# Optimization experiments

Measured on AMD Instinct MI355X. Metric: run time of the kernel, lower is better.

Reference implementation:

```python
import jax, jax.numpy as jnp
import numpy as np

D_MODEL = 1024
D_STATE = 16
D_CONV = 4
EXPAND = 2
D_INNER = D_MODEL * EXPAND
LN_EPS = 1e-5


def setup_inputs() -> dict:
    key = jax.random.key(0)
    ks = jax.random.split(key, 12)
    s = lambda fan_in: 1.0 / np.sqrt(fan_in)
    return {
        "x": jax.random.normal(ks[0], (4, 2048, D_MODEL), dtype=jnp.float32),
        "ln_w": jnp.ones((D_MODEL,), jnp.float32),
        "ln_b": jnp.zeros((D_MODEL,), jnp.float32),
        "W_in": jax.random.uniform(ks[1], (D_MODEL, 2 * D_INNER), jnp.float32, -s(D_MODEL), s(D_MODEL)),
        "b_in": jax.random.uniform(ks[2], (2 * D_INNER,), jnp.float32, -s(D_MODEL), s(D_MODEL)),
        "conv_w": jax.random.uniform(ks[3], (D_INNER, 1, D_CONV), jnp.float32, -s(D_CONV), s(D_CONV)),
        "conv_b": jax.random.uniform(ks[4], (D_INNER,), jnp.float32, -s(D_CONV), s(D_CONV)),
        "A_log": jax.random.normal(ks[5], (D_INNER, D_STATE), jnp.float32),
        "D": jax.random.normal(ks[6], (D_INNER,), jnp.float32),
        "W_x": jax.random.uniform(ks[7], (D_INNER, 2 * D_STATE), jnp.float32, -s(D_INNER), s(D_INNER)),
        "b_x": jax.random.uniform(ks[8], (2 * D_STATE,), jnp.float32, -s(D_INNER), s(D_INNER)),
        "W_out": jax.random.uniform(ks[9], (D_INNER, D_MODEL), jnp.float32, -s(D_INNER), s(D_INNER)),
        "b_out": jax.random.uniform(ks[10], (D_MODEL,), jnp.float32, -s(D_INNER), s(D_INNER)),
    }


def _selective_scan(xc, deltaA, Bm, Cm):
    # xc: (b, s, di), deltaA: (di, n), Bm/Cm: (b, s, n)
    b, _, di = xc.shape
    n = Bm.shape[-1]
    h0 = jnp.zeros((b, di, n), xc.dtype)

    def step(h, inp):
        xt, bt, ct = inp  # (b,di), (b,n), (b,n)
        h = deltaA[None] * h + xt[:, :, None] * bt[:, None, :]
        y = jnp.einsum('bin,bn->bi', h, ct)
        return h, y

    xs = (jnp.swapaxes(xc, 0, 1), jnp.swapaxes(Bm, 0, 1), jnp.swapaxes(Cm, 0, 1))
    _, ys = jax.lax.scan(step, h0, xs)  # ys: (s, b, di)
    return jnp.swapaxes(ys, 0, 1)


def reference(x, ln_w, ln_b, W_in, b_in, conv_w, conv_b, A_log, D, W_x, b_x, W_out, b_out):
    residual = x
    mu = jnp.mean(x, -1, keepdims=True)
    var = jnp.mean((x - mu) ** 2, -1, keepdims=True)
    xn = (x - mu) * jax.lax.rsqrt(var + LN_EPS) * ln_w + ln_b
    xg = xn @ W_in + b_in
    x_main, gate = jnp.split(xg, 2, axis=-1)  # (b,s,di) each
    # causal depthwise conv1d (left pad d_conv-1 == torch pad both + slice [:s])
    xt = jnp.swapaxes(x_main, 1, 2)  # (b, di, s)
    xc = jax.lax.conv_general_dilated(
        xt, conv_w, window_strides=(1,), padding=[(D_CONV - 1, 0)],
        feature_group_count=D_INNER, dimension_numbers=('NCH', 'OIH', 'NCH'))
    xc = xc + conv_b[None, :, None]
    x_conv = jax.nn.silu(jnp.swapaxes(xc, 1, 2))  # (b,s,di)
    ssm = x_conv @ W_x + b_x
    Bm, Cm = jnp.split(ssm, 2, axis=-1)  # (b,s,n)
    deltaA = jnp.exp(-jnp.exp(A_log))  # exp(A), A = -exp(A_log)
    y = _selective_scan(x_conv, deltaA, Bm, Cm)
    y = y + x_conv * D[None, None, :]
    y = y * jax.nn.silu(gate)
    out = y @ W_out + b_out
    return out + residual
```

## Files before the change

### kernel.cpp

```cpp
#include <hip/hip_runtime.h>
#include <stdint.h>

typedef unsigned short u16;
typedef short bf16x8 __attribute__((ext_vector_type(8)));
typedef float f32x4 __attribute__((ext_vector_type(4)));

#define TOKENS 8192
#define SEQ 2048
#define DM 1024
#define DI 2048
#define NCH 32
#define CLEN 64

__device__ __forceinline__ float bf2f(u16 u) {
  union { uint32_t i; float f; } v; v.i = ((uint32_t)u) << 16; return v.f;
}
__device__ __forceinline__ u16 f2bf(float f) {
  union { float f; uint32_t i; } v; v.f = f;
  uint32_t r = v.i + 0x7FFFu + ((v.i >> 16) & 1u);
  return (u16)(r >> 16);
}

__device__ __forceinline__ void g2lds16(const void* g, void* l) {
  __builtin_amdgcn_global_load_lds(
      (const __attribute__((address_space(1))) uint32_t*)g,
      (__attribute__((address_space(3))) uint32_t*)l, 16, 0, 0);
}

__global__ __launch_bounds__(256)
void transpose_to_bf16(const float* __restrict__ src, u16* __restrict__ dst,
                       int R, int C) {
  __shared__ float tile[64][65];
  const int i = threadIdx.x;
  const int tilesC = C >> 6;
  const int br = blockIdx.x / tilesC, bc = blockIdx.x % tilesC;
  const int r0 = br << 6, c0 = bc << 6;
  const int cx = (i & 15) << 2, ry = i >> 4;
#pragma unroll
  for (int p = 0; p < 4; ++p) {
    int row = ry + p * 16;
    float4 v = *(const float4*)&src[(size_t)(r0 + row) * C + c0 + cx];
    tile[row][cx + 0] = v.x; tile[row][cx + 1] = v.y;
    tile[row][cx + 2] = v.z; tile[row][cx + 3] = v.w;
  }
  __syncthreads();
#pragma unroll
  for (int p = 0; p < 4; ++p) {
    int cr = ry + p * 16;
    ushort4 o;
    o.x = f2bf(tile[cx + 0][cr]); o.y = f2bf(tile[cx + 1][cr]);
    o.z = f2bf(tile[cx + 2][cr]); o.w = f2bf(tile[cx + 3][cr]);
    *(ushort4*)&dst[(size_t)(c0 + cr) * R + r0 + cx] = o;
  }
}

__global__ __launch_bounds__(256)
void txpose_wx(const float* __restrict__ src, u16* __restrict__ dst) {
  const int gid = blockIdx.x * 256 + threadIdx.x;
  const int k = gid >> 5, n = gid & 31;
  dst[(size_t)n * DI + k] = f2bf(src[gid]);
}

__global__ __launch_bounds__(256)
void layernorm_bf16(const float* __restrict__ x, const float* __restrict__ lw,
                    const float* __restrict__ lb, u16* __restrict__ xn) {
  const int row = blockIdx.x, tid = threadIdx.x;
  const float4 v = *(const float4*)&x[(size_t)row * DM + tid * 4];
  float s = v.x + v.y + v.z + v.w;
  float q = v.x * v.x + v.y * v.y + v.z * v.z + v.w * v.w;
#pragma unroll
  for (int m = 1; m < 64; m <<= 1) { s += __shfl_xor(s, m); q += __shfl_xor(q, m); }
  __shared__ float red[8];
  const int w = tid >> 6, lane = tid & 63;
  if (lane == 0) { red[w] = s; red[4 + w] = q; }
  __syncthreads();
  s = red[0] + red[1] + red[2] + red[3];
  q = red[4] + red[5] + red[6] + red[7];
  const float mu = s * (1.f / DM);
  const float var = q * (1.f / DM) - mu * mu;
  const float rs = rsqrtf(var + 1e-5f);
  const float4 wv = *(const float4*)&lw[tid * 4];
  const float4 bv = *(const float4*)&lb[tid * 4];
  ushort4 o;
  o.x = f2bf((v.x - mu) * rs * wv.x + bv.x);
  o.y = f2bf((v.y - mu) * rs * wv.y + bv.y);
  o.z = f2bf((v.z - mu) * rs * wv.z + bv.z);
  o.w = f2bf((v.w - mu) * rs * wv.w + bv.w);
  *(ushort4*)&xn[(size_t)row * DM + tid * 4] = o;
}

template <int EPI>
__global__ __launch_bounds__(256)
void gemm_bt(const u16* __restrict__ A, const u16* __restrict__ Bt,
             const float* __restrict__ bias, const float* __restrict__ resid,
             void* __restrict__ out, int M, int N, int K) {
  __shared__ __align__(16) u16 As[128 * 64];
  __shared__ __align__(16) u16 Bs[128 * 64];
  const int tid = threadIdx.x, w = tid >> 6, lane = tid & 63;
  const int ntiles = N >> 7;
  const int tm = blockIdx.x / ntiles, tn = blockIdx.x % ntiles;
  const int m0 = tm << 7, n0 = tn << 7;
  f32x4 acc[4][4];
#pragma unroll
  for (int mi = 0; mi < 4; ++mi)
#pragma unroll
    for (int ni = 0; ni < 4; ++ni) acc[mi][ni] = (f32x4){0.f, 0.f, 0.f, 0.f};

  const int chunkbase = w * 64 + lane;
  const int wm = (w >> 1) * 64, wn = (w & 1) * 64;
  const int fr = lane & 15, fg = lane >> 4;

  for (int kt = 0; kt < K; kt += 64) {
#pragma unroll
    for (int i = 0; i < 4; ++i) {
      int ch = chunkbase + i * 256;
      int row = ch >> 3, c16 = ch & 7;
      g2lds16(A + (size_t)(m0 + row) * K + kt + c16 * 8,
              (u16*)As + (size_t)(w * 64 + i * 256) * 8);
      g2lds16(Bt + (size_t)(n0 + row) * K + kt + c16 * 8,
              (u16*)Bs + (size_t)(w * 64 + i * 256) * 8);
    }
    __syncthreads();
#pragma unroll
    for (int ks = 0; ks < 2; ++ks) {
      bf16x8 af[4], bfr[4];
#pragma unroll
      for (int mi = 0; mi < 4; ++mi)
        af[mi] = *(const bf16x8*)&As[(wm + mi * 16 + fr) * 64 + ks * 32 + fg * 8];
#pragma unroll
      for (int ni = 0; ni < 4; ++ni)
        bfr[ni] = *(const bf16x8*)&Bs[(wn + ni * 16 + fr) * 64 + ks * 32 + fg * 8];
#pragma unroll
      for (int mi = 0; mi < 4; ++mi)
#pragma unroll
        for (int ni = 0; ni < 4; ++ni)
          acc[mi][ni] = __builtin_amdgcn_mfma_f32_16x16x32_bf16(
              af[mi], bfr[ni], acc[mi][ni], 0, 0, 0);
    }
    __syncthreads();
  }
#pragma unroll
  for (int mi = 0; mi < 4; ++mi)
#pragma unroll
    for (int ni = 0; ni < 4; ++ni) {
      const int col = n0 + wn + ni * 16 + fr;
      const float bcol = bias[col];
#pragma unroll
      for (int j = 0; j < 4; ++j) {
        const int row = m0 + wm + mi * 16 + fg * 4 + j;
        float v = acc[mi][ni][j] + bcol;
        if (EPI == 1) {
          ((float*)out)[(size_t)row * N + col] = v + resid[(size_t)row * N + col];
        } else {
          ((u16*)out)[(size_t)row * N + col] = f2bf(v);
        }
      }
    }
}

__global__ __launch_bounds__(256)
void conv_silu(const u16* __restrict__ xg, const float* __restrict__ cw,
               const float* __restrict__ cb, u16* __restrict__ xconv) {
  const int t = blockIdx.x;
  const int s = t & (SEQ - 1);
  const int d = threadIdx.x * 8;
  float xv[4][8];
#pragma unroll
  for (int j = 0; j < 4; ++j) {
    const int ss = s - 3 + j;
    if (ss >= 0) {
      uint4 u = *(const uint4*)&xg[(size_t)(t - 3 + j) * (2 * DI) + d];
      const u16* pu = (const u16*)&u;
#pragma unroll
      for (int q = 0; q < 8; ++q) xv[j][q] = bf2f(pu[q]);
    } else {
#pragma unroll
      for (int q = 0; q < 8; ++q) xv[j][q] = 0.f;
    }
  }
  u16 outp[8];
#pragma unroll
  for (int q = 0; q < 8; ++q) {
    const float4 wq = *(const float4*)&cw[(d + q) * 4];
    float a = cb[d + q] + wq.x * xv[0][q] + wq.y * xv[1][q] + wq.z * xv[2][q] +
              wq.w * xv[3][q];
    outp[q] = f2bf(a / (1.f + __expf(-a)));
  }
  *(uint4*)&xconv[(size_t)t * DI + d] = *(const uint4*)outp;
}

__global__ __launch_bounds__(256)
void bc_gemm(const u16* __restrict__ xconv, const u16* __restrict__ wxT,
             float* __restrict__ BCp) {
  __shared__ __align__(16) u16 As[128 * 64];
  __shared__ __align__(16) u16 Bs[32 * 64];
  const int tid = threadIdx.x, w = tid >> 6, lane = tid & 63;
  const int mt = blockIdx.x & 63;
  const int ks_id = blockIdx.x >> 6;
  const int m0 = mt << 7;
  const int k0 = ks_id << 9;
  const int fr = lane & 15, fg = lane >> 4;
  f32x4 acc[2][2];
#pragma unroll
  for (int mf = 0; mf < 2; ++mf)
#pragma unroll
    for (int nf = 0; nf < 2; ++nf) acc[mf][nf] = (f32x4){0.f, 0.f, 0.f, 0.f};

  for (int kt = k0; kt < k0 + 512; kt += 64) {
#pragma unroll
    for (int i = 0; i < 4; ++i) {
      int ch = w * 64 + lane + i * 256;
      int row = ch >> 3, c16 = ch & 7;
      g2lds16(xconv + (size_t)(m0 + row) * DI + kt + c16 * 8,
              (u16*)As + (size_t)(w * 64 + i * 256) * 8);
    }
    {
      int row = tid >> 3, c16 = tid & 7;
      g2lds16(wxT + (size_t)row * DI + kt + c16 * 8,
              (u16*)Bs + (size_t)(w * 64) * 8);
    }
    __syncthreads();
#pragma unroll
    for (int ks = 0; ks < 2; ++ks) {
      bf16x8 af[2], bfr[2];
#pragma unroll
      for (int mf = 0; mf < 2; ++mf)
        af[mf] = *(const bf16x8*)&As[(w * 32 + mf * 16 + fr) * 64 + ks * 32 + fg * 8];
#pragma unroll
      for (int nf = 0; nf < 2; ++nf)
        bfr[nf] = *(const bf16x8*)&Bs[(nf * 16 + fr) * 64 + ks * 32 + fg * 8];
#pragma unroll
      for (int mf = 0; mf < 2; ++mf)
#pragma unroll
        for (int nf = 0; nf < 2; ++nf)
          acc[mf][nf] = __builtin_amdgcn_mfma_f32_16x16x32_bf16(
              af[mf], bfr[nf], acc[mf][nf], 0, 0, 0);
    }
    __syncthreads();
  }
#pragma unroll
  for (int mf = 0; mf < 2; ++mf)
#pragma unroll
    for (int nf = 0; nf < 2; ++nf) {
      const int col = nf * 16 + fr;
#pragma unroll
      for (int j = 0; j < 4; ++j) {
        const int row = m0 + w * 32 + mf * 16 + fg * 4 + j;
        BCp[((size_t)ks_id * TOKENS + row) * 32 + col] = acc[mf][nf][j];
      }
    }
}

__global__ __launch_bounds__(256)
void bc_reduce(const float* __restrict__ BCp, const float* __restrict__ bx,
               float* __restrict__ BC) {
  const int gid = blockIdx.x * 256 + threadIdx.x;
  const int c = gid & 31;
  const size_t t = gid >> 5;
  float s = bx[c] + BCp[t * 32 + c] + BCp[((size_t)TOKENS + t) * 32 + c] +
            BCp[((size_t)2 * TOKENS + t) * 32 + c] +
            BCp[((size_t)3 * TOKENS + t) * 32 + c];
  const int dc = (c < 16) ? 2 * c : 2 * (c - 16) + 1;
  BC[t * 32 + dc] = s;
}

__global__ __launch_bounds__(256)
void scan_passA(const u16* __restrict__ xconv, const float* __restrict__ BC,
                const float* __restrict__ A_log, float* __restrict__ F) {
  __shared__ float bcs[CLEN * 32];
  const int blk = blockIdx.x;
  const int j = blk & (NCH - 1);
  const int dg = (blk >> 5) & 7;
  const int b = blk >> 8;
  const int tid = threadIdx.x;
  const int d = dg * 256 + tid;
  const int t0 = j * CLEN;
  {
    const float4* s4 = (const float4*)(BC + (size_t)(b * SEQ + t0) * 32);
    float4* d4 = (float4*)bcs;
#pragma unroll
    for (int i = 0; i < 2; ++i) d4[tid + i * 256] = s4[tid + i * 256];
  }
  float dA[16], h[16];
#pragma unroll
  for (int n = 0; n < 16; ++n) {
    dA[n] = __expf(-__expf(A_log[d * 16 + n]));
    h[n] = 0.f;
  }
  __syncthreads();
  const u16* xcp = xconv + (size_t)(b * SEQ + t0) * DI + d;
  for (int t = 0; t < CLEN; ++t) {
    const float xc = bf2f(*xcp);
    xcp += DI;
#pragma unroll
    for (int n = 0; n < 16; ++n)
      h[n] = fmaf(dA[n], h[n], xc * bcs[t * 32 + 2 * n]);
  }
  float* fp = F + ((size_t)((b * NCH + j) * DI) + d) * 16;
#pragma unroll
  for (int n = 0; n < 16; n += 4) {
    float4 v = {h[n], h[n + 1], h[n + 2], h[n + 3]};
    *(float4*)&fp[n] = v;
  }
}

__global__ __launch_bounds__(256)
void scan_passB(const float* __restrict__ A_log, float* __restrict__ F) {
  const int gid = blockIdx.x * 256 + threadIdx.x;
  const int n = gid & 15;
  const int d = (gid >> 4) & (DI - 1);
  const int b = gid >> 15;
  const float dAL = __expf(-(float)CLEN * __expf(A_log[d * 16 + n]));
  float carry = 0.f;
  const size_t base = ((size_t)(b * NCH) * DI + d) * 16 + n;
  const size_t stride = (size_t)DI * 16;
  for (int j = 0; j < NCH; ++j) {
    const size_t idx = base + (size_t)j * stride;
    const float f = F[idx];
    F[idx] = carry;
    carry = fmaf(dAL, carry, f);
  }
}

__global__ __launch_bounds__(256)
void scan_passC(const u16* __restrict__ xconv, const u16* __restrict__ xg,
                const float* __restrict__ BC, const float* __restrict__ A_log,
                const float* __restrict__ Dv, const float* __restrict__ F,
                u16* __restrict__ yact) {
  __shared__ float bcs[CLEN * 32];
  const int blk = blockIdx.x;
  const int j = blk & (NCH - 1);
  const int dg = (blk >> 5) & 7;
  const int b = blk >> 8;
  const int tid = threadIdx.x;
  const int d = dg * 256 + tid;
  const int t0 = j * CLEN;
  {
    const float4* s4 = (const float4*)(BC + (size_t)(b * SEQ + t0) * 32);
    float4* d4 = (float4*)bcs;
#pragma unroll
    for (int i = 0; i < 2; ++i) d4[tid + i * 256] = s4[tid + i * 256];
  }
  float dA[16], h[16];
  const float* fp = F + ((size_t)((b * NCH + j) * DI) + d) * 16;
#pragma unroll
  for (int n = 0; n < 16; n += 4) {
    float4 v = *(const float4*)&fp[n];
    h[n] = v.x; h[n + 1] = v.y; h[n + 2] = v.z; h[n + 3] = v.w;
  }
#pragma unroll
  for (int n = 0; n < 16; ++n) dA[n] = __expf(-__expf(A_log[d * 16 + n]));
  const float Dd = Dv[d];
  __syncthreads();
  const u16* xcp = xconv + (size_t)(b * SEQ + t0) * DI + d;
  const u16* gp = xg + (size_t)(b * SEQ + t0) * (2 * DI) + DI + d;
  u16* yp = yact + (size_t)(b * SEQ + t0) * DI + d;
  for (int t = 0; t < CLEN; ++t) {
    const float xc = bf2f(*xcp);
    const float g = bf2f(*gp);
    float y0 = 0.f, y1 = 0.f, y2 = 0.f, y3 = 0.f;
#pragma unroll
    for (int n = 0; n < 16; n += 4) {
      h[n]     = fmaf(dA[n],     h[n],     xc * bcs[t * 32 + 2 * n]);
      y0 = fmaf(bcs[t * 32 + 2 * n + 1], h[n], y0);
      h[n + 1] = fmaf(dA[n + 1], h[n + 1], xc * bcs[t * 32 + 2 * n + 2]);
      y1 = fmaf(bcs[t * 32 + 2 * n + 3], h[n + 1], y1);
      h[n + 2] = fmaf(dA[n + 2], h[n + 2], xc * bcs[t * 32 + 2 * n + 4]);
      y2 = fmaf(bcs[t * 32 + 2 * n + 5], h[n + 2], y2);
      h[n + 3] = fmaf(dA[n + 3], h[n + 3], xc * bcs[t * 32 + 2 * n + 6]);
      y3 = fmaf(bcs[t * 32 + 2 * n + 7], h[n + 3], y3);
    }
    const float y = (y0 + y1) + (y2 + y3);
    const float ya = (y + xc * Dd) * (g / (1.f + __expf(-g)));
    *yp = f2bf(ya);
    xcp += DI; gp += 2 * DI; yp += DI;
  }
}

extern "C" void kernel_launch(void* const* d_in, const int* in_sizes, int n_in,
                              void* d_out, int out_size, void* d_ws, size_t ws_size,
                              hipStream_t stream) {
  const float* x     = (const float*)d_in[0];
  const float* ln_w  = (const float*)d_in[1];
  const float* ln_b  = (const float*)d_in[2];
  const float* W_in  = (const float*)d_in[3];
  const float* b_in  = (const float*)d_in[4];
  const float* cw    = (const float*)d_in[5];
  const float* cb    = (const float*)d_in[6];
  const float* A_log = (const float*)d_in[7];
  const float* Dv    = (const float*)d_in[8];
  const float* W_x   = (const float*)d_in[9];
  const float* b_x   = (const float*)d_in[10];
  const float* W_out = (const float*)d_in[11];
  const float* b_out = (const float*)d_in[12];

  char* ws = (char*)d_ws;
  size_t off = 0;
  auto alloc = [&](size_t bytes) {
    void* p = ws + off;
    off += (bytes + 255) & ~(size_t)255;
    return p;
  };
  u16* WinT  = (u16*)alloc((size_t)(2 * DI) * DM * 2);
  u16* WoutT = (u16*)alloc((size_t)DM * DI * 2);
  u16* xn    = (u16*)alloc((size_t)TOKENS * DM * 2);
  u16* xg    = (u16*)alloc((size_t)TOKENS * (2 * DI) * 2);
  u16* xconv = (u16*)alloc((size_t)TOKENS * DI * 2);
  float* BC  = (float*)alloc((size_t)TOKENS * 32 * 4);
  u16* yact  = (u16*)alloc((size_t)TOKENS * DI * 2);
  u16* WxT   = (u16*)alloc((size_t)32 * DI * 2);
  float* BCp = (float*)alloc((size_t)4 * TOKENS * 32 * 4);
  float* F   = (float*)xn;
  (void)ws_size; (void)in_sizes; (void)n_in; (void)out_size;

  transpose_to_bf16<<<(DM / 64) * ((2 * DI) / 64), 256, 0, stream>>>(W_in, WinT, DM, 2 * DI);
  transpose_to_bf16<<<(DI / 64) * (DM / 64), 256, 0, stream>>>(W_out, WoutT, DI, DM);
  txpose_wx<<<(DI * 32) / 256, 256, 0, stream>>>(W_x, WxT);
  layernorm_bf16<<<TOKENS, 256, 0, stream>>>(x, ln_w, ln_b, xn);
  gemm_bt<0><<<(TOKENS / 128) * ((2 * DI) / 128), 256, 0, stream>>>(
      xn, WinT, b_in, nullptr, xg, TOKENS, 2 * DI, DM);
  conv_silu<<<TOKENS, 256, 0, stream>>>(xg, cw, cb, xconv);
  bc_gemm<<<256, 256, 0, stream>>>(xconv, WxT, BCp);
  bc_reduce<<<(TOKENS * 32) / 256, 256, 0, stream>>>(BCp, b_x, BC);
  scan_passA<<<4 * 8 * NCH, 256, 0, stream>>>(xconv, BC, A_log, F);
  scan_passB<<<512, 256, 0, stream>>>(A_log, F);
  scan_passC<<<4 * 8 * NCH, 256, 0, stream>>>(xconv, xg, BC, A_log, Dv, F, yact);
  gemm_bt<1><<<(TOKENS / 128) * (DM / 128), 256, 0, stream>>>(
      yact, WoutT, b_out, x, d_out, TOKENS, DM, DI);
}
```

Measured before the change: 428.8 us.

## Rewrite bf16 GEMM with triple-buffered LDS pipeline, 128x256 tiles and swizzle

Replaces the single-buffered 128x128 GEMM with a 512-thread 128x256 tile kernel that prefetches three K-stages into LDS via async global-to-LDS loads, using explicit vmcnt waits and barriers. It adds an XOR swizzle on LDS columns to avoid bank conflicts, block-index remapping across XCDs for L2 locality, and setprio around the MFMA section. The goal is to hide global load latency behind MFMA work and raise arithmetic intensity, at the cost of large LDS use (about 144KB) that limits the kernel to one block per CU.

```diff
diff --git a/kernel.cpp b/kernel.cpp
--- a/kernel.cpp
+++ b/kernel.cpp
@@ -89,56 +89,94 @@
   *(ushort4*)&xn[(size_t)row * DM + tid * 4] = o;
 }
 
+#define TILE_U16 ((128 + 256) * 64)
 template <int EPI>
-__global__ __launch_bounds__(256)
-void gemm_bt(const u16* __restrict__ A, const u16* __restrict__ Bt,
-             const float* __restrict__ bias, const float* __restrict__ resid,
-             void* __restrict__ out, int M, int N, int K) {
-  __shared__ __align__(16) u16 As[128 * 64];
-  __shared__ __align__(16) u16 Bs[128 * 64];
-  const int tid = threadIdx.x, w = tid >> 6, lane = tid & 63;
-  const int ntiles = N >> 7;
-  const int tm = blockIdx.x / ntiles, tn = blockIdx.x % ntiles;
-  const int m0 = tm << 7, n0 = tn << 7;
+__global__ __launch_bounds__(512, 1)
+void gemm3(const u16* __restrict__ A, const u16* __restrict__ Bt,
+           const float* __restrict__ bias, const float* __restrict__ resid,
+           void* __restrict__ out, int M, int N, int K) {
+  __shared__ __align__(16) u16 lds[3 * TILE_U16];
+  const int tid = threadIdx.x, wid = tid >> 6, lane = tid & 63;
+  const int ntiles = N >> 8;
+  int bid = blockIdx.x;
+  {
+    const int cpx = gridDim.x >> 3;
+    bid = (bid & 7) * cpx + (bid >> 3);
+  }
+  const int tm = bid / ntiles, tn = bid % ntiles;
+  const int m0 = tm << 7, n0 = tn << 8;
+  const int wm = (wid >> 2) * 64, wn = (wid & 3) * 64;
+  const int fr = lane & 15, fg = lane >> 4;
+  const int c0 = (fg ^ (fr & 7)) << 4;
+  const int NK = K >> 6;
+
   f32x4 acc[4][4];
 #pragma unroll
   for (int mi = 0; mi < 4; ++mi)
 #pragma unroll
     for (int ni = 0; ni < 4; ++ni) acc[mi][ni] = (f32x4){0.f, 0.f, 0.f, 0.f};
 
-  const int chunkbase = w * 64 + lane;
-  const int wm = (w >> 1) * 64, wn = (w & 1) * 64;
-  const int fr = lane & 15, fg = lane >> 4;
-
-  for (int kt = 0; kt < K; kt += 64) {
+  auto stage = [&](int T) {
+    const int kt = T << 6;
+    u16* buf = lds + (T % 3) * TILE_U16;
+#pragma unroll
+    for (int i = 0; i < 2; ++i) {
+      const int s = i * 512 + tid;
+      const int row = s >> 3, l = (s & 7) ^ (row & 7);
+      g2lds16(A + (size_t)(m0 + row) * K + kt + l * 8, buf + s * 8);
+    }
+    u16* bufB = buf + 128 * 64;
 #pragma unroll
     for (int i = 0; i < 4; ++i) {
-      int ch = chunkbase + i * 256;
-      int row = ch >> 3, c16 = ch & 7;
-      g2lds16(A + (size_t)(m0 + row) * K + kt + c16 * 8,
-              (u16*)As + (size_t)(w * 64 + i * 256) * 8);
-      g2lds16(Bt + (size_t)(n0 + row) * K + kt + c16 * 8,
-              (u16*)Bs + (size_t)(w * 64 + i * 256) * 8);
-    }
-    __syncthreads();
+      const int s = i * 512 + tid;
+      const int row = s >> 3, l = (s & 7) ^ (row & 7);
+      g2lds16(Bt + (size_t)(n0 + row) * K + kt + l * 8, bufB + s * 8);
+    }
+  };
+
+  stage(0); stage(1); stage(2);
+  asm volatile("s_waitcnt vmcnt(12)" ::: "memory");
+  __builtin_amdgcn_s_barrier();
+  asm volatile("" ::: "memory");
+
+  for (int T = 0; T < NK; ++T) {
+    const char* bufA = (const char*)(lds + (T % 3) * TILE_U16);
+    const char* bufB = bufA + 128 * 64 * 2;
+    bf16x8 af[2][4], bf_[2][4];
 #pragma unroll
     for (int ks = 0; ks < 2; ++ks) {
-      bf16x8 af[4], bfr[4];
+      const int cb = c0 ^ (ks << 6);
 #pragma unroll
       for (int mi = 0; mi < 4; ++mi)
-        af[mi] = *(const bf16x8*)&As[(wm + mi * 16 + fr) * 64 + ks * 32 + fg * 8];
+        af[ks][mi] = *(const bf16x8*)(bufA + (wm + mi * 16 + fr) * 128 + cb);
 #pragma unroll
       for (int ni = 0; ni < 4; ++ni)
-        bfr[ni] = *(const bf16x8*)&Bs[(wn + ni * 16 + fr) * 64 + ks * 32 + fg * 8];
+        bf_[ks][ni] = *(const bf16x8*)(bufB + (wn + ni * 16 + fr) * 128 + cb);
+    }
+    __builtin_amdgcn_s_setprio(1);
+#pragma unroll
+    for (int ks = 0; ks < 2; ++ks)
 #pragma unroll
       for (int mi = 0; mi < 4; ++mi)
 #pragma unroll
         for (int ni = 0; ni < 4; ++ni)
           acc[mi][ni] = __builtin_amdgcn_mfma_f32_16x16x32_bf16(
-              af[mi], bfr[ni], acc[mi][ni], 0, 0, 0);
-    }
-    __syncthreads();
-  }
+              af[ks][mi], bf_[ks][ni], acc[mi][ni], 0, 0, 0);
+    __builtin_amdgcn_s_setprio(0);
+    __builtin_amdgcn_s_barrier();
+    asm volatile("" ::: "memory");
+    if (T + 3 < NK) {
+      stage(T + 3);
+      asm volatile("s_waitcnt vmcnt(12)" ::: "memory");
+    } else if (T + 2 < NK) {
+      asm volatile("s_waitcnt vmcnt(6)" ::: "memory");
+    } else if (T + 1 < NK) {
+      asm volatile("s_waitcnt vmcnt(0)" ::: "memory");
+    }
+    __builtin_amdgcn_s_barrier();
+    asm volatile("" ::: "memory");
+  }
+
 #pragma unroll
   for (int mi = 0; mi < 4; ++mi)
 #pragma unroll
@@ -417,7 +455,7 @@
   transpose_to_bf16<<<(DI / 64) * (DM / 64), 256, 0, stream>>>(W_out, WoutT, DI, DM);
   txpose_wx<<<(DI * 32) / 256, 256, 0, stream>>>(W_x, WxT);
   layernorm_bf16<<<TOKENS, 256, 0, stream>>>(x, ln_w, ln_b, xn);
-  gemm_bt<0><<<(TOKENS / 128) * ((2 * DI) / 128), 256, 0, stream>>>(
+  gemm3<0><<<(TOKENS / 128) * ((2 * DI) / 256), 512, 0, stream>>>(
       xn, WinT, b_in, nullptr, xg, TOKENS, 2 * DI, DM);
   conv_silu<<<TOKENS, 256, 0, stream>>>(xg, cw, cb, xconv);
   bc_gemm<<<256, 256, 0, stream>>>(xconv, WxT, BCp);
@@ -425,6 +463,6 @@
   scan_passA<<<4 * 8 * NCH, 256, 0, stream>>>(xconv, BC, A_log, F);
   scan_passB<<<512, 256, 0, stream>>>(A_log, F);
   scan_passC<<<4 * 8 * NCH, 256, 0, stream>>>(xconv, xg, BC, A_log, Dv, F, yact);
-  gemm_bt<1><<<(TOKENS / 128) * (DM / 128), 256, 0, stream>>>(
+  gemm3<1><<<(TOKENS / 128) * (DM / 256), 512, 0, stream>>>(
       yact, WoutT, b_out, x, d_out, TOKENS, DM, DI);
 }
```

Result: faster. 413.3 us (-3.6%).
